# Optimization experiments

Hardware: AMD Instinct MI355X
Metric: run time of the kernel (lower is better)

Reference implementation:

```python
import jax, jax.numpy as jnp
from jax import lax
import numpy as np

N, H, K, B, L = 8192, 256, 100, 32, 128
FS = [1, 2, 3, 4]
W2 = 2 * H + 10  # conv kernel width; padded input width (2H+10) == kernel width -> out width 1


def setup_inputs() -> dict:
    key = jax.random.key(0)
    ks = jax.random.split(key, 16)
    inp = {}
    # scale adj by 1/sqrt(N) so layer1 activations stay O(1) (keeps softmax numerically sane)
    inp["adj"] = jax.random.normal(ks[0], (N, N), jnp.float32) / np.float32(np.sqrt(N))
    # xavier-uniform-scale init for the node embedding parameter
    inp["embedding"] = jax.random.normal(ks[1], (N, H), jnp.float32) * np.float32(np.sqrt(2.0 / (N + H)))
    inp["q_idx"] = jax.random.randint(ks[2], (B, L), 0, N, dtype=jnp.int32)
    inp["a_idx"] = jax.random.randint(ks[3], (B, L), 0, N, dtype=jnp.int32)
    for i, fs in enumerate(FS):
        fan_in = fs * W2
        inp[f"conv_w{i}"] = jax.random.normal(ks[4 + i], (K, 1, fs, W2), jnp.float32) / np.float32(np.sqrt(fan_in))
        inp[f"conv_b{i}"] = jnp.zeros((K,), jnp.float32)
    inp["dense_w"] = jax.random.normal(ks[12], (4 * K * 2, 2), jnp.float32) * np.float32(0.02)
    inp["dense_b"] = jnp.zeros((2,), jnp.float32)
    return inp


def _cnn_branch(t, conv_ws, conv_bs):
    # t: [B, 1, L, 2H]; each conv has padding=5 on both spatial dims,
    # kernel width == 2H+10 so output width == 1; relu then max-pool over full height.
    outs = []
    for w, b in zip(conv_ws, conv_bs):
        y = lax.conv_general_dilated(t, w, (1, 1), [(5, 5), (5, 5)],
                                     dimension_numbers=("NCHW", "OIHW", "NCHW"))
        y = jax.nn.relu(y + b[None, :, None, None])  # [B, K, L+10-fs+1, 1]
        outs.append(jnp.max(y, axis=(2, 3)))  # [B, K]
    return jnp.concatenate(outs, axis=1)  # [B, 4K]


def reference(adj, embedding, q_idx, a_idx,
              conv_w0, conv_b0, conv_w1, conv_b1,
              conv_w2, conv_b2, conv_w3, conv_b3,
              dense_w, dense_b):
    conv_ws = [conv_w0, conv_w1, conv_w2, conv_w3]
    conv_bs = [conv_b0, conv_b1, conv_b2, conv_b3]
    # featureless GCN layer: layer1 = A @ E  -> [N, H]
    layer1 = adj @ embedding
    # per-sample word gathers (ragged in original, fixed length L here)
    Q = layer1[q_idx]  # [B, L, H]
    A = layer1[a_idx]  # [B, L, H]
    # soft alignment: score = Q A^T; wq = softmax rows; wa = softmax(score.T, dim=1) == softmax over axis 1
    score = jnp.einsum("blh,bmh->blm", Q, A)
    wq = jax.nn.softmax(score, axis=2)
    wa = jax.nn.softmax(score, axis=1)
    EQ = jnp.einsum("blm,bmh->blh", wq, A)  # aligned encoding of Q
    EA = jnp.einsum("blm,blh->bmh", wa, Q)  # aligned encoding of A
    # match features: squared diff ++ elementwise product -> [B, 1, L, 2H]
    tq = jnp.concatenate([(Q - EQ) ** 2, Q * EQ], axis=-1)[:, None]
    ta = jnp.concatenate([(A - EA) ** 2, A * EA], axis=-1)[:, None]
    # dropout is identity in eval mode
    q_re = jax.nn.relu(_cnn_branch(tq, conv_ws, conv_bs))  # [B, 4K]
    a_re = jax.nn.relu(_cnn_branch(ta, conv_ws, conv_bs))  # [B, 4K]
    re = jnp.concatenate([q_re, a_re], axis=1)  # [B, 8K]
    logits = re @ dense_w + dense_b  # [B, 2]  (F.relu(score) in original is a discarded no-op)
    return jax.nn.log_softmax(logits, axis=1)
```

## Files before the change

### kernel.cpp

```cpp
#include <hip/hip_runtime.h>
#include <hip/hip_bf16.h>
#include <stdint.h>

typedef unsigned short u16;
typedef __attribute__((ext_vector_type(8))) short bf16x8;
typedef __attribute__((ext_vector_type(4))) float f32x4;

#define NN 8192
#define HH 256
#define KK 100
#define BB 32
#define LL 128
#define NPAD 1024
#define SPLITK 8
#define KCH (NN / SPLITK)
#define STEPS1 (KCH / 64)
#define STEPS2 (512 / 64)

__device__ __forceinline__ u16 f2bf_rne(float x) {
  union { __hip_bfloat16 h; u16 u; } v;
  v.h = __float2bfloat16(x);
  return v.u;
}

__device__ __forceinline__ float bf2f(u16 u) {
  union { unsigned int i; float f; } v;
  v.i = ((unsigned int)u) << 16;
  return v.f;
}

__device__ __forceinline__ bf16x8 pack8(f32x4 a, f32x4 b) {
  bf16x8 r;
  r[0] = (short)f2bf_rne(a.x); r[1] = (short)f2bf_rne(a.y);
  r[2] = (short)f2bf_rne(a.z); r[3] = (short)f2bf_rne(a.w);
  r[4] = (short)f2bf_rne(b.x); r[5] = (short)f2bf_rne(b.y);
  r[6] = (short)f2bf_rne(b.z); r[7] = (short)f2bf_rne(b.w);
  return r;
}

__device__ __forceinline__ void gld16(const void* g, void* l) {
  __builtin_amdgcn_global_load_lds(
      (const __attribute__((address_space(1))) unsigned int*)g,
      (__attribute__((address_space(3))) unsigned int*)l, 16, 0, 0);
}

__global__ __launch_bounds__(256) void convert_embT(const float* __restrict__ emb,
                                                    u16* __restrict__ embT) {
  __shared__ float t[64][65];
  const int tid = threadIdx.x;
  const int k0 = blockIdx.x * 64, n0 = blockIdx.y * 64;
#pragma unroll
  for (int i = 0; i < 16; ++i) {
    int idx = i * 256 + tid;
    int r = idx >> 6, c = idx & 63;
    t[r][c] = emb[(size_t)(k0 + r) * HH + n0 + c];
  }
  __syncthreads();
#pragma unroll
  for (int i = 0; i < 16; ++i) {
    int idx = i * 256 + tid;
    int r = idx >> 6, c = idx & 63;
    embT[(size_t)(n0 + r) * NN + k0 + c] = f2bf_rne(t[c][r]);
  }
}

__global__ __launch_bounds__(1024) void dedup_rows(const int* __restrict__ q_idx,
                                                   const int* __restrict__ a_idx,
                                                   int* __restrict__ rank,
                                                   int* __restrict__ rows,
                                                   int* __restrict__ muniq) {
  __shared__ unsigned bm[256];
  __shared__ int cnt[1024];
  __shared__ int total;
  const int tid = threadIdx.x;
  if (tid < 256) bm[tid] = 0u;
  __syncthreads();
  for (int i = tid; i < BB * LL; i += 1024) {
    int q = q_idx[i];
    atomicOr(&bm[q >> 5], 1u << (q & 31));
  }
  for (int i = tid; i < BB * LL; i += 1024) {
    int a = a_idx[i];
    atomicOr(&bm[a >> 5], 1u << (a & 31));
  }
  __syncthreads();
  const unsigned w = bm[tid >> 2];
  const unsigned byte = (w >> ((tid & 3) * 8)) & 0xffu;
  const int myc = __popc(byte);
  cnt[tid] = myc;
  __syncthreads();
  for (int off = 1; off < 1024; off <<= 1) {
    int v = (tid >= off) ? cnt[tid - off] : 0;
    __syncthreads();
    cnt[tid] += v;
    __syncthreads();
  }
  if (tid == 1023) total = cnt[1023];
  int base = cnt[tid] - myc;
#pragma unroll
  for (int j = 0; j < 8; ++j) {
    int n = tid * 8 + j;
    int bit = (byte >> j) & 1;
    rank[n] = base;
    if (bit) rows[base++] = n;
  }
  __syncthreads();
  if (tid == 0) *muniq = total;
  if (tid < 128) rows[total + tid] = 0;
}

__global__ __launch_bounds__(512, 6) void gemm_layer1c(const float* __restrict__ adj,
                                                       const u16* __restrict__ embT,
                                                       const int* __restrict__ rows,
                                                       const int* __restrict__ muniq,
                                                       u16* __restrict__ parts) {
  __shared__ __align__(16) float As[64 * 64];
  __shared__ __align__(16) u16 Bs[256 * 64];
  const int tid = threadIdx.x;
  const int lane = tid & 63, wid = tid >> 6;
  const int wm = wid >> 2, wn = wid & 3;
  const int wg = blockIdx.x;
  const int sk = wg & 7;
  const int mt = wg >> 3;
  const int m0 = mt * 64;
  const int M = *muniq;
  if (m0 >= M) return;
  const int kbeg = sk * KCH;

  f32x4 acc[2][4];
  const f32x4 zf = {0.f, 0.f, 0.f, 0.f};
#pragma unroll
  for (int i = 0; i < 2; ++i)
#pragma unroll
    for (int j = 0; j < 4; ++j) acc[i][j] = zf;

  int aRowLoc[2], aGsrc[2];
  const float* aSrc[2];
#pragma unroll
  for (int j = 0; j < 2; ++j) {
    int t = wid * 2 + j;
    aRowLoc[j] = t * 4 + (lane >> 4);
    aGsrc[j] = (lane & 15) ^ (aRowLoc[j] & 15);
    int grow = rows[m0 + aRowLoc[j]];
    aSrc[j] = adj + (size_t)grow * NN + kbeg + aGsrc[j] * 4;
  }
  const u16* bSrc[4];
#pragma unroll
  for (int j = 0; j < 4; ++j) {
    int t = wid * 4 + j;
    int rowB = t * 8 + (lane >> 3);
    int g = (lane & 7) ^ (rowB & 7);
    bSrc[j] = embT + (size_t)rowB * NN + kbeg + g * 8;
  }

  for (int s = 0; s < STEPS1; ++s) {
    const int ks = s * 64;
#pragma unroll
    for (int j = 0; j < 2; ++j)
      gld16(aSrc[j] + ks, (void*)&As[(wid * 2 + j) * 256]);
#pragma unroll
    for (int j = 0; j < 4; ++j)
      gld16(bSrc[j] + ks, (void*)&Bs[(wid * 4 + j) * 512]);
    __syncthreads();
#pragma unroll
    for (int kk = 0; kk < 64; kk += 32) {
      bf16x8 af[2], bfr[4];
      const int g0 = (kk >> 2) + ((lane >> 4) << 1);
#pragma unroll
      for (int mi = 0; mi < 2; ++mi) {
        int row = wm * 32 + mi * 16 + (lane & 15);
        f32x4 p0 = *reinterpret_cast<const f32x4*>(&As[row * 64 + ((g0 ^ (row & 15)) << 2)]);
        f32x4 p1 = *reinterpret_cast<const f32x4*>(&As[row * 64 + (((g0 + 1) ^ (row & 15)) << 2)]);
        af[mi] = pack8(p0, p1);
      }
      const int gb = (kk >> 3) + (lane >> 4);
#pragma unroll
      for (int ni = 0; ni < 4; ++ni) {
        int row = wn * 64 + ni * 16 + (lane & 15);
        bfr[ni] = *reinterpret_cast<const bf16x8*>(&Bs[row * 64 + ((gb ^ (row & 7)) << 3)]);
      }
#pragma unroll
      for (int mi = 0; mi < 2; ++mi)
#pragma unroll
        for (int ni = 0; ni < 4; ++ni)
          acc[mi][ni] = __builtin_amdgcn_mfma_f32_16x16x32_bf16(af[mi], bfr[ni], acc[mi][ni], 0, 0, 0);
    }
    __syncthreads();
  }

  u16* outp = parts + (size_t)sk * ((size_t)NN * HH);
  const int r0 = (lane >> 4) << 2;
  const int coln = wn * 64 + (lane & 15);
#pragma unroll
  for (int mi = 0; mi < 2; ++mi)
#pragma unroll
    for (int ni = 0; ni < 4; ++ni)
#pragma unroll
      for (int r = 0; r < 4; ++r)
        outp[(size_t)(m0 + wm * 32 + mi * 16 + r0 + r) * HH + coln + ni * 16] = f2bf_rne(acc[mi][ni][r]);
}

__global__ __launch_bounds__(256) void gather_qa(const u16* __restrict__ parts,
                                                 const int* __restrict__ q_idx,
                                                 const int* __restrict__ a_idx,
                                                 const int* __restrict__ rank,
                                                 u16* __restrict__ Qbf, u16* __restrict__ Abf) {
  const int rb = blockIdx.x;
  const bool isA = rb >= BB * LL;
  const int r = isA ? rb - BB * LL : rb;
  const int idx = (isA ? a_idx : q_idx)[r];
  const int cidx = rank[idx];
  const int tid = threadIdx.x;
  float s = 0.f;
#pragma unroll
  for (int p = 0; p < SPLITK; ++p)
    s += bf2f(parts[(size_t)p * ((size_t)NN * HH) + (size_t)cidx * HH + tid]);
  (isA ? Abf : Qbf)[(size_t)r * HH + tid] = f2bf_rne(s);
}

__global__ __launch_bounds__(512) void attn_fused(const u16* __restrict__ Qbf,
                                                  const u16* __restrict__ Abf,
                                                  u16* __restrict__ wqbf,
                                                  u16* __restrict__ watbf) {
  __shared__ __align__(16) char lraw[131072];
  u16* Qs = (u16*)lraw;
  u16* As = (u16*)(lraw + 65536);
  float* sc = (float*)lraw;
  const int b = blockIdx.x;
  const int tid = threadIdx.x;
  const int lane = tid & 63, wid = tid >> 6;
  const int wm = wid >> 2, wn = wid & 3;

  const u16* qsrc = Qbf + (size_t)b * (LL * HH);
  const u16* asrc = Abf + (size_t)b * (LL * HH);
#pragma unroll
  for (int i = 0; i < 8; ++i) {
    int gf = i * 512 + tid;
    int l = gf >> 5, g = gf & 31;
    int gp = g ^ (l & 7);
    *reinterpret_cast<bf16x8*>(&Qs[l * 256 + gp * 8]) = *reinterpret_cast<const bf16x8*>(qsrc + l * 256 + g * 8);
    *reinterpret_cast<bf16x8*>(&As[l * 256 + gp * 8]) = *reinterpret_cast<const bf16x8*>(asrc + l * 256 + g * 8);
  }
  __syncthreads();

  f32x4 acc[4][2];
  const f32x4 zf = {0.f, 0.f, 0.f, 0.f};
#pragma unroll
  for (int i = 0; i < 4; ++i)
#pragma unroll
    for (int j = 0; j < 2; ++j) acc[i][j] = zf;

#pragma unroll
  for (int ks = 0; ks < 8; ++ks) {
    bf16x8 af[4], bfr[2];
#pragma unroll
    for (int mi = 0; mi < 4; ++mi) {
      int row = wm * 64 + mi * 16 + (lane & 15);
      int g = ks * 4 + (lane >> 4);
      af[mi] = *reinterpret_cast<const bf16x8*>(&Qs[row * 256 + (g ^ (row & 7)) * 8]);
    }
#pragma unroll
    for (int ni = 0; ni < 2; ++ni) {
      int row = wn * 32 + ni * 16 + (lane & 15);
      int g = ks * 4 + (lane >> 4);
      bfr[ni] = *reinterpret_cast<const bf16x8*>(&As[row * 256 + (g ^ (row & 7)) * 8]);
    }
#pragma unroll
    for (int mi = 0; mi < 4; ++mi)
#pragma unroll
      for (int ni = 0; ni < 2; ++ni)
        acc[mi][ni] = __builtin_amdgcn_mfma_f32_16x16x32_bf16(af[mi], bfr[ni], acc[mi][ni], 0, 0, 0);
  }
  __syncthreads();

  const int r0 = (lane >> 4) << 2;
#pragma unroll
  for (int mi = 0; mi < 4; ++mi)
#pragma unroll
    for (int ni = 0; ni < 2; ++ni) {
      int m = wn * 32 + ni * 16 + (lane & 15);
#pragma unroll
      for (int r = 0; r < 4; ++r) {
        int l = wm * 64 + mi * 16 + r0 + r;
        sc[l * 132 + m] = acc[mi][ni][r];
      }
    }
  __syncthreads();

  {
    const int l = tid >> 2, j = tid & 3;
    const int base = l * 132 + j * 32;
    float mx = -3.4e38f;
#pragma unroll 8
    for (int c = 0; c < 32; ++c) mx = fmaxf(mx, sc[base + c]);
    mx = fmaxf(mx, __shfl_xor(mx, 1));
    mx = fmaxf(mx, __shfl_xor(mx, 2));
    float sum = 0.f;
#pragma unroll 8
    for (int c = 0; c < 32; ++c) sum += expf(sc[base + c] - mx);
    sum += __shfl_xor(sum, 1);
    sum += __shfl_xor(sum, 2);
    float inv = 1.f / sum;
    u16* o = wqbf + (size_t)b * (LL * LL) + l * 128 + j * 32;
#pragma unroll 8
    for (int c = 0; c < 32; ++c) o[c] = f2bf_rne(expf(sc[base + c] - mx) * inv);
  }
  {
    const int m = tid >> 2, j = tid & 3;
    float mx = -3.4e38f;
#pragma unroll 8
    for (int r = 0; r < 32; ++r) mx = fmaxf(mx, sc[(j * 32 + r) * 132 + m]);
    mx = fmaxf(mx, __shfl_xor(mx, 1));
    mx = fmaxf(mx, __shfl_xor(mx, 2));
    float sum = 0.f;
#pragma unroll 8
    for (int r = 0; r < 32; ++r) sum += expf(sc[(j * 32 + r) * 132 + m] - mx);
    sum += __shfl_xor(sum, 1);
    sum += __shfl_xor(sum, 2);
    float inv = 1.f / sum;
    u16* o = watbf + (size_t)b * (LL * LL) + m * 128 + j * 32;
#pragma unroll 8
    for (int r = 0; r < 32; ++r) o[r] = f2bf_rne(expf(sc[(j * 32 + r) * 132 + m] - mx) * inv);
  }
}

__global__ __launch_bounds__(512) void align_mfma(const u16* __restrict__ wqbf,
                                                  const u16* __restrict__ watbf,
                                                  const u16* __restrict__ Qbf,
                                                  const u16* __restrict__ Abf,
                                                  u16* __restrict__ Tbf) {
  __shared__ __align__(16) u16 wsh[128 * 128];
  __shared__ __align__(16) u16 srcT[256 * 140];
  const int bid = blockIdx.x;
  const int side = bid >> 5, b = bid & 31;
  const int tid = threadIdx.x;
  const int lane = tid & 63, wid = tid >> 6;
  const int wm = wid >> 2, wn = wid & 3;

  const u16* wsrc = (side ? watbf : wqbf) + (size_t)b * (LL * LL);
  const u16* ssrc = (side ? Qbf : Abf) + (size_t)b * (LL * HH);
  const u16* msrc = (side ? Abf : Qbf) + (size_t)b * (LL * HH);

#pragma unroll
  for (int i = 0; i < 4; ++i) {
    int gf = i * 512 + tid;
    int row = gf >> 4, g = gf & 15;
    int gp = g ^ (row & 7);
    *reinterpret_cast<bf16x8*>(&wsh[row * 128 + gp * 8]) = *reinterpret_cast<const bf16x8*>(wsrc + row * 128 + g * 8);
  }
#pragma unroll
  for (int i = 0; i < 8; ++i) {
    int gf = i * 512 + tid;
    int j = gf >> 5, g = gf & 31;
    bf16x8 v = *reinterpret_cast<const bf16x8*>(ssrc + j * 256 + g * 8);
#pragma unroll
    for (int e = 0; e < 8; ++e) srcT[(g * 8 + e) * 140 + j] = (u16)v[e];
  }
  __syncthreads();

  f32x4 acc[4][4];
  const f32x4 zf = {0.f, 0.f, 0.f, 0.f};
#pragma unroll
  for (int i = 0; i < 4; ++i)
#pragma unroll
    for (int j = 0; j < 4; ++j) acc[i][j] = zf;

#pragma unroll
  for (int ks = 0; ks < 4; ++ks) {
    bf16x8 af[4], bfr[4];
#pragma unroll
    for (int mi = 0; mi < 4; ++mi) {
      int row = wm * 64 + mi * 16 + (lane & 15);
      int g = ks * 4 + (lane >> 4);
      af[mi] = *reinterpret_cast<const bf16x8*>(&wsh[row * 128 + (g ^ (row & 7)) * 8]);
    }
#pragma unroll
    for (int ni = 0; ni < 4; ++ni) {
      int h = wn * 64 + ni * 16 + (lane & 15);
      int k = ks * 32 + ((lane >> 4) << 3);
      bfr[ni] = *reinterpret_cast<const bf16x8*>(&srcT[h * 140 + k]);
    }
#pragma unroll
    for (int mi = 0; mi < 4; ++mi)
#pragma unroll
      for (int ni = 0; ni < 4; ++ni)
        acc[mi][ni] = __builtin_amdgcn_mfma_f32_16x16x32_bf16(af[mi], bfr[ni], acc[mi][ni], 0, 0, 0);
  }

  u16* outp = Tbf + (size_t)(side * 4096 + b * 128) * 512;
  const int r0 = (lane >> 4) << 2;
#pragma unroll
  for (int mi = 0; mi < 4; ++mi)
#pragma unroll
    for (int ni = 0; ni < 4; ++ni) {
      int h = wn * 64 + ni * 16 + (lane & 15);
#pragma unroll
      for (int r = 0; r < 4; ++r) {
        int i2 = wm * 64 + mi * 16 + r0 + r;
        float mv = bf2f(msrc[(size_t)i2 * HH + h]);
        float e = acc[mi][ni][r];
        float d = mv - e;
        outp[(size_t)i2 * 512 + h] = f2bf_rne(d * d);
        outp[(size_t)i2 * 512 + 256 + h] = f2bf_rne(mv * e);
      }
    }
}

__global__ __launch_bounds__(256) void prep_wcat(const float* __restrict__ w0,
                                                 const float* __restrict__ w1,
                                                 const float* __restrict__ w2,
                                                 const float* __restrict__ w3,
                                                 u16* __restrict__ Wcat) {
  const int kr = blockIdx.x;
  const int tid = threadIdx.x;
  u16* out = Wcat + (size_t)kr * 512;
  if (kr >= KK * 10) {
    out[tid] = 0;
    out[tid + 256] = 0;
    return;
  }
  const int k = kr / 10, s = kr % 10;
  const float* w;
  int r, fs;
  if (s < 1)      { w = w0; r = s;     fs = 1; }
  else if (s < 3) { w = w1; r = s - 1; fs = 2; }
  else if (s < 6) { w = w2; r = s - 3; fs = 3; }
  else            { w = w3; r = s - 6; fs = 4; }
  const float* src = w + ((size_t)k * fs + r) * 522 + 5;
  out[tid] = f2bf_rne(src[tid]);
  out[tid + 256] = f2bf_rne(src[tid + 256]);
}

__global__ __launch_bounds__(512, 4) void gemm_conv(const u16* __restrict__ Tbf,
                                                    const u16* __restrict__ Wcat,
                                                    u16* __restrict__ D) {
  __shared__ __align__(16) u16 As[128 * 64];
  __shared__ __align__(16) u16 Bs[256 * 64];
  const int tid = threadIdx.x;
  const int lane = tid & 63, wid = tid >> 6;
  const int wm = wid >> 2, wn = wid & 3;
  const int m0 = blockIdx.x * 128;
  const int n0 = blockIdx.y * 256;

  f32x4 acc[4][4];
  const f32x4 zf = {0.f, 0.f, 0.f, 0.f};
#pragma unroll
  for (int i = 0; i < 4; ++i)
#pragma unroll
    for (int j = 0; j < 4; ++j) acc[i][j] = zf;

  const int browL = (lane >> 3);
  const int bkL = (lane & 7) << 3;

  for (int s = 0; s < STEPS2; ++s) {
    const int ks = s * 64;
#pragma unroll
    for (int j = 0; j < 2; ++j) {
      int rowA = (wid << 4) + (j << 3) + browL;
      int kA = bkL ^ ((rowA & 7) << 3);
      gld16(Tbf + (size_t)(m0 + rowA) * 512 + ks + kA, (void*)&As[(wid * 2 + j) * 512]);
    }
#pragma unroll
    for (int j = 0; j < 4; ++j) {
      int rowB = (wid << 5) + (j << 3) + browL;
      int kB = bkL ^ ((rowB & 7) << 3);
      gld16(Wcat + (size_t)(n0 + rowB) * 512 + ks + kB, (void*)&Bs[(wid * 4 + j) * 512]);
    }
    __syncthreads();
#pragma unroll
    for (int kk = 0; kk < 64; kk += 32) {
      const int krow = kk + ((lane >> 4) << 3);
      bf16x8 af[4], bfr[4];
#pragma unroll
      for (int mi = 0; mi < 4; ++mi) {
        int row = wm * 64 + mi * 16 + (lane & 15);
        af[mi] = *reinterpret_cast<const bf16x8*>(&As[row * 64 + (krow ^ ((row & 7) << 3))]);
      }
#pragma unroll
      for (int ni = 0; ni < 4; ++ni) {
        int row = wn * 64 + ni * 16 + (lane & 15);
        bfr[ni] = *reinterpret_cast<const bf16x8*>(&Bs[row * 64 + (krow ^ ((row & 7) << 3))]);
      }
#pragma unroll
      for (int mi = 0; mi < 4; ++mi)
#pragma unroll
        for (int ni = 0; ni < 4; ++ni)
          acc[mi][ni] = __builtin_amdgcn_mfma_f32_16x16x32_bf16(af[mi], bfr[ni], acc[mi][ni], 0, 0, 0);
    }
    __syncthreads();
  }

  const int r0 = (lane >> 4) << 2;
  const int coln = n0 + wn * 64 + (lane & 15);
#pragma unroll
  for (int mi = 0; mi < 4; ++mi)
#pragma unroll
    for (int ni = 0; ni < 4; ++ni)
#pragma unroll
      for (int r = 0; r < 4; ++r)
        D[(size_t)(m0 + wm * 64 + mi * 16 + r0 + r) * NPAD + coln + ni * 16] = f2bf_rne(acc[mi][ni][r]);
}

__global__ __launch_bounds__(256) void reduce_conv(const u16* __restrict__ D,
                                                   const float* __restrict__ b0,
                                                   const float* __restrict__ b1,
                                                   const float* __restrict__ b2,
                                                   const float* __restrict__ b3,
                                                   float* __restrict__ re) {
  __shared__ float tile[128][101];
  const int pair = blockIdx.y;
  const int sel = pair >> 5, b = pair & 31;
  const int kc = blockIdx.x;
  const int tid = threadIdx.x;
  const int rowbase = sel * (BB * LL) + b * LL;
  const int c0 = kc * 100;
  for (int idx = tid; idx < 12800; idx += 256) {
    int r = idx / 100, c = idx - r * 100;
    tile[r][c] = bf2f(D[(size_t)(rowbase + r) * NPAD + c0 + c]);
  }
  __syncthreads();
  const int wid = tid >> 6, lane = tid & 63;
  const int offt[4] = {0, 1, 3, 6};
  const int fst[4] = {1, 2, 3, 4};
  for (int o = wid; o < 40; o += 4) {
    const int kk = o >> 2, f = o & 3;
    const int fs = fst[f], off = offt[f];
    const int kg = kc * 10 + kk;
    const float bias = (f == 0 ? b0 : f == 1 ? b1 : f == 2 ? b2 : b3)[kg];
    const int col = kk * 10 + off;
    const int outh = 139 - fs;
    float best = 0.f;
    for (int i = lane; i < outh; i += 64) {
      float s = bias;
#pragma unroll 4
      for (int r = 0; r < 4; ++r) {
        if (r < fs) {
          int j = i + r - 5;
          if (j >= 0 && j < LL) s += tile[j][col + r];
        }
      }
      best = fmaxf(best, s);
    }
    best = fmaxf(best, 0.f);
#pragma unroll
    for (int d = 32; d; d >>= 1) best = fmaxf(best, __shfl_xor(best, d));
    if (lane == 0) re[(size_t)b * 800 + sel * 400 + f * 100 + kg] = best;
  }
}

__global__ __launch_bounds__(64) void dense_logsm(const float* __restrict__ re,
                                                  const float* __restrict__ dw,
                                                  const float* __restrict__ db,
                                                  float* __restrict__ out) {
  const int b = blockIdx.x;
  const int lane = threadIdx.x;
  const float* r = re + (size_t)b * 800;
  float a0 = 0.f, a1 = 0.f;
  for (int j = lane; j < 800; j += 64) {
    float rv = r[j];
    a0 += rv * dw[j * 2];
    a1 += rv * dw[j * 2 + 1];
  }
#pragma unroll
  for (int d = 32; d; d >>= 1) {
    a0 += __shfl_xor(a0, d);
    a1 += __shfl_xor(a1, d);
  }
  if (lane == 0) {
    a0 += db[0];
    a1 += db[1];
    float mx = fmaxf(a0, a1);
    float lse = mx + logf(expf(a0 - mx) + expf(a1 - mx));
    out[b * 2] = a0 - lse;
    out[b * 2 + 1] = a1 - lse;
  }
}

static const size_t OFF_PARTS = 0;
static const size_t OFF_D     = 0;
static const size_t OFF_QBF   = 67108864;
static const size_t OFF_ABF   = OFF_QBF + 2097152;
static const size_t OFF_WQB   = OFF_ABF + 2097152;
static const size_t OFF_WAB   = OFF_WQB + 1048576;
static const size_t OFF_RE    = OFF_WAB + 1048576;
static const size_t OFF_TBF   = OFF_RE + 102400;
static const size_t OFF_WCAT  = OFF_TBF + 8388608;
static const size_t OFF_EMBT  = OFF_WCAT + 1048576;
static const size_t OFF_RANK  = OFF_EMBT + 4194304;
static const size_t OFF_ROWS  = OFF_RANK + 32768;
static const size_t OFF_MUNIQ = OFF_ROWS + 33280;

extern "C" void kernel_launch(void* const* d_in, const int* in_sizes, int n_in,
                              void* d_out, int out_size, void* d_ws, size_t ws_size,
                              hipStream_t stream) {
  (void)in_sizes; (void)n_in; (void)out_size; (void)ws_size;
  const float* adj  = (const float*)d_in[0];
  const float* emb  = (const float*)d_in[1];
  const int* q_idx  = (const int*)d_in[2];
  const int* a_idx  = (const int*)d_in[3];
  const float* cw0 = (const float*)d_in[4];
  const float* cb0 = (const float*)d_in[5];
  const float* cw1 = (const float*)d_in[6];
  const float* cb1 = (const float*)d_in[7];
  const float* cw2 = (const float*)d_in[8];
  const float* cb2 = (const float*)d_in[9];
  const float* cw3 = (const float*)d_in[10];
  const float* cb3 = (const float*)d_in[11];
  const float* dw = (const float*)d_in[12];
  const float* db = (const float*)d_in[13];
  float* out = (float*)d_out;

  char* ws = (char*)d_ws;
  u16* parts   = (u16*)(ws + OFF_PARTS);
  u16* Dbuf    = (u16*)(ws + OFF_D);
  u16* Qbf     = (u16*)(ws + OFF_QBF);
  u16* Abf     = (u16*)(ws + OFF_ABF);
  u16* wqbf    = (u16*)(ws + OFF_WQB);
  u16* watbf   = (u16*)(ws + OFF_WAB);
  float* re    = (float*)(ws + OFF_RE);
  u16* Tbf     = (u16*)(ws + OFF_TBF);
  u16* Wcat    = (u16*)(ws + OFF_WCAT);
  u16* embT    = (u16*)(ws + OFF_EMBT);
  int* rank    = (int*)(ws + OFF_RANK);
  int* rows    = (int*)(ws + OFF_ROWS);
  int* muniq   = (int*)(ws + OFF_MUNIQ);

  convert_embT<<<dim3(128, 4), 256, 0, stream>>>(emb, embT);
  dedup_rows<<<1, 1024, 0, stream>>>(q_idx, a_idx, rank, rows, muniq);
  prep_wcat<<<1024, 256, 0, stream>>>(cw0, cw1, cw2, cw3, Wcat);
  gemm_layer1c<<<128 * SPLITK, 512, 0, stream>>>(adj, embT, rows, muniq, parts);
  gather_qa<<<2 * BB * LL, 256, 0, stream>>>(parts, q_idx, a_idx, rank, Qbf, Abf);
  attn_fused<<<BB, 512, 0, stream>>>(Qbf, Abf, wqbf, watbf);
  align_mfma<<<64, 512, 0, stream>>>(wqbf, watbf, Qbf, Abf, Tbf);
  gemm_conv<<<dim3(64, 4), 512, 0, stream>>>(Tbf, Wcat, Dbuf);
  reduce_conv<<<dim3(10, 64), 256, 0, stream>>>(Dbuf, cb0, cb1, cb2, cb3, re);
  dense_logsm<<<BB, 64, 0, stream>>>(re, dw, db, out);
}
```

Measured before the change: 148.8 us.

## Split layer1 GEMM into 64x128 tiles with 256-thread blocks

The layer1 gather GEMM now splits the 256-wide output into two N-halves, so each block is 4 waves computing a 64x128 tile instead of 8 waves computing 64x256. The grid doubles, and each wave holds a 4x2 MFMA accumulator layout instead of 2x4. This raises block count and cuts LDS per block for better occupancy and load balance. In exchange, every adj A-tile (fp32, the dominant traffic) is now loaded twice, once per N-half.

```diff
diff --git a/kernel.cpp b/kernel.cpp
--- a/kernel.cpp
+++ b/kernel.cpp
@@ -109,40 +109,40 @@
   if (tid < 128) rows[total + tid] = 0;
 }
 
-__global__ __launch_bounds__(512, 6) void gemm_layer1c(const float* __restrict__ adj,
+__global__ __launch_bounds__(256, 5) void gemm_layer1f(const float* __restrict__ adj,
                                                        const u16* __restrict__ embT,
                                                        const int* __restrict__ rows,
                                                        const int* __restrict__ muniq,
                                                        u16* __restrict__ parts) {
   __shared__ __align__(16) float As[64 * 64];
-  __shared__ __align__(16) u16 Bs[256 * 64];
+  __shared__ __align__(16) u16 Bs[128 * 64];
   const int tid = threadIdx.x;
   const int lane = tid & 63, wid = tid >> 6;
-  const int wm = wid >> 2, wn = wid & 3;
   const int wg = blockIdx.x;
   const int sk = wg & 7;
-  const int mt = wg >> 3;
+  const int nt = (wg >> 3) & 1;
+  const int mt = wg >> 4;
   const int m0 = mt * 64;
   const int M = *muniq;
   if (m0 >= M) return;
+  const int n0 = nt * 128;
   const int kbeg = sk * KCH;
 
-  f32x4 acc[2][4];
+  f32x4 acc[4][2];
   const f32x4 zf = {0.f, 0.f, 0.f, 0.f};
 #pragma unroll
-  for (int i = 0; i < 2; ++i)
-#pragma unroll
-    for (int j = 0; j < 4; ++j) acc[i][j] = zf;
-
-  int aRowLoc[2], aGsrc[2];
-  const float* aSrc[2];
-#pragma unroll
-  for (int j = 0; j < 2; ++j) {
-    int t = wid * 2 + j;
-    aRowLoc[j] = t * 4 + (lane >> 4);
-    aGsrc[j] = (lane & 15) ^ (aRowLoc[j] & 15);
-    int grow = rows[m0 + aRowLoc[j]];
-    aSrc[j] = adj + (size_t)grow * NN + kbeg + aGsrc[j] * 4;
+  for (int i = 0; i < 4; ++i)
+#pragma unroll
+    for (int j = 0; j < 2; ++j) acc[i][j] = zf;
+
+  const float* aSrc[4];
+#pragma unroll
+  for (int j = 0; j < 4; ++j) {
+    int t = wid * 4 + j;
+    int rloc = t * 4 + (lane >> 4);
+    int g = (lane & 15) ^ (rloc & 15);
+    int grow = rows[m0 + rloc];
+    aSrc[j] = adj + (size_t)grow * NN + kbeg + g * 4;
   }
   const u16* bSrc[4];
 #pragma unroll
@@ -150,39 +150,38 @@
     int t = wid * 4 + j;
     int rowB = t * 8 + (lane >> 3);
     int g = (lane & 7) ^ (rowB & 7);
-    bSrc[j] = embT + (size_t)rowB * NN + kbeg + g * 8;
+    bSrc[j] = embT + (size_t)(n0 + rowB) * NN + kbeg + g * 8;
   }
 
   for (int s = 0; s < STEPS1; ++s) {
     const int ks = s * 64;
 #pragma unroll
-    for (int j = 0; j < 2; ++j)
-      gld16(aSrc[j] + ks, (void*)&As[(wid * 2 + j) * 256]);
-#pragma unroll
-    for (int j = 0; j < 4; ++j)
+    for (int j = 0; j < 4; ++j) {
+      gld16(aSrc[j] + ks, (void*)&As[(wid * 4 + j) * 256]);
       gld16(bSrc[j] + ks, (void*)&Bs[(wid * 4 + j) * 512]);
+    }
     __syncthreads();
 #pragma unroll
     for (int kk = 0; kk < 64; kk += 32) {
-      bf16x8 af[2], bfr[4];
+      bf16x8 af[4], bfr[2];
       const int g0 = (kk >> 2) + ((lane >> 4) << 1);
 #pragma unroll
-      for (int mi = 0; mi < 2; ++mi) {
-        int row = wm * 32 + mi * 16 + (lane & 15);
+      for (int mi = 0; mi < 4; ++mi) {
+        int row = mi * 16 + (lane & 15);
         f32x4 p0 = *reinterpret_cast<const f32x4*>(&As[row * 64 + ((g0 ^ (row & 15)) << 2)]);
         f32x4 p1 = *reinterpret_cast<const f32x4*>(&As[row * 64 + (((g0 + 1) ^ (row & 15)) << 2)]);
         af[mi] = pack8(p0, p1);
       }
       const int gb = (kk >> 3) + (lane >> 4);
 #pragma unroll
-      for (int ni = 0; ni < 4; ++ni) {
-        int row = wn * 64 + ni * 16 + (lane & 15);
+      for (int ni = 0; ni < 2; ++ni) {
+        int row = wid * 32 + ni * 16 + (lane & 15);
         bfr[ni] = *reinterpret_cast<const bf16x8*>(&Bs[row * 64 + ((gb ^ (row & 7)) << 3)]);
       }
 #pragma unroll
-      for (int mi = 0; mi < 2; ++mi)
-#pragma unroll
-        for (int ni = 0; ni < 4; ++ni)
+      for (int mi = 0; mi < 4; ++mi)
+#pragma unroll
+        for (int ni = 0; ni < 2; ++ni)
           acc[mi][ni] = __builtin_amdgcn_mfma_f32_16x16x32_bf16(af[mi], bfr[ni], acc[mi][ni], 0, 0, 0);
     }
     __syncthreads();
@@ -190,14 +189,14 @@
 
   u16* outp = parts + (size_t)sk * ((size_t)NN * HH);
   const int r0 = (lane >> 4) << 2;
-  const int coln = wn * 64 + (lane & 15);
-#pragma unroll
-  for (int mi = 0; mi < 2; ++mi)
-#pragma unroll
-    for (int ni = 0; ni < 4; ++ni)
+  const int coln = n0 + wid * 32 + (lane & 15);
+#pragma unroll
+  for (int mi = 0; mi < 4; ++mi)
+#pragma unroll
+    for (int ni = 0; ni < 2; ++ni)
 #pragma unroll
       for (int r = 0; r < 4; ++r)
-        outp[(size_t)(m0 + wm * 32 + mi * 16 + r0 + r) * HH + coln + ni * 16] = f2bf_rne(acc[mi][ni][r]);
+        outp[(size_t)(m0 + mi * 16 + r0 + r) * HH + coln + ni * 16] = f2bf_rne(acc[mi][ni][r]);
 }
 
 __global__ __launch_bounds__(256) void gather_qa(const u16* __restrict__ parts,
@@ -628,7 +627,7 @@
   convert_embT<<<dim3(128, 4), 256, 0, stream>>>(emb, embT);
   dedup_rows<<<1, 1024, 0, stream>>>(q_idx, a_idx, rank, rows, muniq);
   prep_wcat<<<1024, 256, 0, stream>>>(cw0, cw1, cw2, cw3, Wcat);
-  gemm_layer1c<<<128 * SPLITK, 512, 0, stream>>>(adj, embT, rows, muniq, parts);
+  gemm_layer1f<<<128 * 2 * SPLITK, 256, 0, stream>>>(adj, embT, rows, muniq, parts);
   gather_qa<<<2 * BB * LL, 256, 0, stream>>>(parts, q_idx, a_idx, rank, Qbf, Abf);
   attn_fused<<<BB, 512, 0, stream>>>(Qbf, Abf, wqbf, watbf);
   align_mfma<<<64, 512, 0, stream>>>(wqbf, watbf, Qbf, Abf, Tbf);
```

After: 153.0 us. 1.03x slower.

## Fuse conv GEMM with shift-sum max-pool reduction via shared memory

Applied to the files above, without the earlier changes.

Merges the conv GEMM and the reduction kernel into one. Each block now computes one 128-row sample tile against a 160-column slice of weights (16 filters × 10 taps), writes the bf16 result into shared memory, and does the shifted row-sum, bias, relu and max-pool in place. This removes the global round-trip of the intermediate D buffer and one kernel launch. In exchange the tile shape changes to 128×160, the grid grows to 448 blocks, and the weight matrix is padded to 1120 rows, so some padded columns are computed and then discarded.

```diff
diff --git a/kernel.cpp b/kernel.cpp
--- a/kernel.cpp
+++ b/kernel.cpp
@@ -11,11 +11,10 @@
 #define KK 100
 #define BB 32
 #define LL 128
-#define NPAD 1024
 #define SPLITK 8
 #define KCH (NN / SPLITK)
 #define STEPS1 (KCH / 64)
-#define STEPS2 (512 / 64)
+#define WCATR 1120
 
 __device__ __forceinline__ u16 f2bf_rne(float x) {
   union { __hip_bfloat16 h; u16 u; } v;
@@ -431,103 +430,94 @@
   out[tid + 256] = f2bf_rne(src[tid + 256]);
 }
 
-__global__ __launch_bounds__(512, 4) void gemm_conv(const u16* __restrict__ Tbf,
-                                                    const u16* __restrict__ Wcat,
-                                                    u16* __restrict__ D) {
-  __shared__ __align__(16) u16 As[128 * 64];
-  __shared__ __align__(16) u16 Bs[256 * 64];
+__global__ __launch_bounds__(512, 4) void gemm_conv_red(const u16* __restrict__ Tbf,
+                                                        const u16* __restrict__ Wcat,
+                                                        const float* __restrict__ b0,
+                                                        const float* __restrict__ b1,
+                                                        const float* __restrict__ b2,
+                                                        const float* __restrict__ b3,
+                                                        float* __restrict__ re) {
+  __shared__ __align__(16) char smem[41472];
+  u16* As = (u16*)smem;
+  u16* Bs = (u16*)(smem + 16384);
+  u16* Dt = (u16*)smem;
   const int tid = threadIdx.x;
   const int lane = tid & 63, wid = tid >> 6;
-  const int wm = wid >> 2, wn = wid & 3;
-  const int m0 = blockIdx.x * 128;
-  const int n0 = blockIdx.y * 256;
-
-  f32x4 acc[4][4];
+  const int wm = wid >> 1, wn = wid & 1;
+  const int bx = blockIdx.x;
+  const int pair = bx / 7, nt = bx % 7;
+  const int sel = pair >> 5, b = pair & 31;
+  const int m0 = pair * 128;
+  const int n0 = nt * 160;
+
+  f32x4 acc[2][5];
   const f32x4 zf = {0.f, 0.f, 0.f, 0.f};
 #pragma unroll
-  for (int i = 0; i < 4; ++i)
-#pragma unroll
-    for (int j = 0; j < 4; ++j) acc[i][j] = zf;
-
-  const int browL = (lane >> 3);
-  const int bkL = (lane & 7) << 3;
-
-  for (int s = 0; s < STEPS2; ++s) {
+  for (int i = 0; i < 2; ++i)
+#pragma unroll
+    for (int j = 0; j < 5; ++j) acc[i][j] = zf;
+
+  for (int s = 0; s < 8; ++s) {
     const int ks = s * 64;
 #pragma unroll
     for (int j = 0; j < 2; ++j) {
-      int rowA = (wid << 4) + (j << 3) + browL;
-      int kA = bkL ^ ((rowA & 7) << 3);
-      gld16(Tbf + (size_t)(m0 + rowA) * 512 + ks + kA, (void*)&As[(wid * 2 + j) * 512]);
-    }
-#pragma unroll
-    for (int j = 0; j < 4; ++j) {
-      int rowB = (wid << 5) + (j << 3) + browL;
-      int kB = bkL ^ ((rowB & 7) << 3);
-      gld16(Wcat + (size_t)(n0 + rowB) * 512 + ks + kB, (void*)&Bs[(wid * 4 + j) * 512]);
+      int t = wid * 2 + j;
+      int rowA = t * 8 + (lane >> 3);
+      int kA = ((lane & 7) ^ (rowA & 7)) << 3;
+      gld16(Tbf + (size_t)(m0 + rowA) * 512 + ks + kA, (void*)&As[t * 512]);
+    }
+    for (int t = wid; t < 20; t += 8) {
+      int rowB = t * 8 + (lane >> 3);
+      int kB = ((lane & 7) ^ (rowB & 7)) << 3;
+      gld16(Wcat + (size_t)(n0 + rowB) * 512 + ks + kB, (void*)&Bs[t * 512]);
     }
     __syncthreads();
 #pragma unroll
     for (int kk = 0; kk < 64; kk += 32) {
-      const int krow = kk + ((lane >> 4) << 3);
-      bf16x8 af[4], bfr[4];
-#pragma unroll
-      for (int mi = 0; mi < 4; ++mi) {
-        int row = wm * 64 + mi * 16 + (lane & 15);
-        af[mi] = *reinterpret_cast<const bf16x8*>(&As[row * 64 + (krow ^ ((row & 7) << 3))]);
+      const int k8 = (kk >> 3) + (lane >> 4);
+      bf16x8 af[2], bfr[5];
+#pragma unroll
+      for (int mi = 0; mi < 2; ++mi) {
+        int row = wm * 32 + mi * 16 + (lane & 15);
+        af[mi] = *reinterpret_cast<const bf16x8*>(&As[row * 64 + ((k8 ^ (row & 7)) << 3)]);
       }
 #pragma unroll
-      for (int ni = 0; ni < 4; ++ni) {
-        int row = wn * 64 + ni * 16 + (lane & 15);
-        bfr[ni] = *reinterpret_cast<const bf16x8*>(&Bs[row * 64 + (krow ^ ((row & 7) << 3))]);
+      for (int ni = 0; ni < 5; ++ni) {
+        int row = wn * 80 + ni * 16 + (lane & 15);
+        bfr[ni] = *reinterpret_cast<const bf16x8*>(&Bs[row * 64 + ((k8 ^ (row & 7)) << 3)]);
       }
 #pragma unroll
-      for (int mi = 0; mi < 4; ++mi)
-#pragma unroll
-        for (int ni = 0; ni < 4; ++ni)
+      for (int mi = 0; mi < 2; ++mi)
+#pragma unroll
+        for (int ni = 0; ni < 5; ++ni)
           acc[mi][ni] = __builtin_amdgcn_mfma_f32_16x16x32_bf16(af[mi], bfr[ni], acc[mi][ni], 0, 0, 0);
     }
     __syncthreads();
   }
 
   const int r0 = (lane >> 4) << 2;
-  const int coln = n0 + wn * 64 + (lane & 15);
-#pragma unroll
-  for (int mi = 0; mi < 4; ++mi)
-#pragma unroll
-    for (int ni = 0; ni < 4; ++ni)
+#pragma unroll
+  for (int mi = 0; mi < 2; ++mi)
+#pragma unroll
+    for (int ni = 0; ni < 5; ++ni) {
+      int col = wn * 80 + ni * 16 + (lane & 15);
 #pragma unroll
       for (int r = 0; r < 4; ++r)
-        D[(size_t)(m0 + wm * 64 + mi * 16 + r0 + r) * NPAD + coln + ni * 16] = f2bf_rne(acc[mi][ni][r]);
-}
-
-__global__ __launch_bounds__(256) void reduce_conv(const u16* __restrict__ D,
-                                                   const float* __restrict__ b0,
-                                                   const float* __restrict__ b1,
-                                                   const float* __restrict__ b2,
-                                                   const float* __restrict__ b3,
-                                                   float* __restrict__ re) {
-  __shared__ float tile[128][101];
-  const int pair = blockIdx.y;
-  const int sel = pair >> 5, b = pair & 31;
-  const int kc = blockIdx.x;
-  const int tid = threadIdx.x;
-  const int rowbase = sel * (BB * LL) + b * LL;
-  const int c0 = kc * 100;
-  for (int idx = tid; idx < 12800; idx += 256) {
-    int r = idx / 100, c = idx - r * 100;
-    tile[r][c] = bf2f(D[(size_t)(rowbase + r) * NPAD + c0 + c]);
-  }
-  __syncthreads();
-  const int wid = tid >> 6, lane = tid & 63;
+        Dt[(wm * 32 + mi * 16 + r0 + r) * 162 + col] = f2bf_rne(acc[mi][ni][r]);
+    }
+  __syncthreads();
+
   const int offt[4] = {0, 1, 3, 6};
   const int fst[4] = {1, 2, 3, 4};
-  for (int o = wid; o < 40; o += 4) {
-    const int kk = o >> 2, f = o & 3;
+#pragma unroll
+  for (int oi = 0; oi < 8; ++oi) {
+    const int o = wid * 8 + oi;
+    const int kl = o >> 2, f = o & 3;
+    const int kglob = nt * 16 + kl;
+    if (kglob >= KK) continue;
     const int fs = fst[f], off = offt[f];
-    const int kg = kc * 10 + kk;
-    const float bias = (f == 0 ? b0 : f == 1 ? b1 : f == 2 ? b2 : b3)[kg];
-    const int col = kk * 10 + off;
+    const float bias = (f == 0 ? b0 : f == 1 ? b1 : f == 2 ? b2 : b3)[kglob];
+    const int col = kl * 10 + off;
     const int outh = 139 - fs;
     float best = 0.f;
     for (int i = lane; i < outh; i += 64) {
@@ -536,7 +526,7 @@
       for (int r = 0; r < 4; ++r) {
         if (r < fs) {
           int j = i + r - 5;
-          if (j >= 0 && j < LL) s += tile[j][col + r];
+          if (j >= 0 && j < LL) s += bf2f(Dt[j * 162 + col + r]);
         }
       }
       best = fmaxf(best, s);
@@ -544,7 +534,7 @@
     best = fmaxf(best, 0.f);
 #pragma unroll
     for (int d = 32; d; d >>= 1) best = fmaxf(best, __shfl_xor(best, d));
-    if (lane == 0) re[(size_t)b * 800 + sel * 400 + f * 100 + kg] = best;
+    if (lane == 0) re[(size_t)b * 800 + sel * 400 + f * 100 + kglob] = best;
   }
 }
 
@@ -577,7 +567,6 @@
 }
 
 static const size_t OFF_PARTS = 0;
-static const size_t OFF_D     = 0;
 static const size_t OFF_QBF   = 67108864;
 static const size_t OFF_ABF   = OFF_QBF + 2097152;
 static const size_t OFF_WQB   = OFF_ABF + 2097152;
@@ -585,7 +574,7 @@
 static const size_t OFF_RE    = OFF_WAB + 1048576;
 static const size_t OFF_TBF   = OFF_RE + 102400;
 static const size_t OFF_WCAT  = OFF_TBF + 8388608;
-static const size_t OFF_EMBT  = OFF_WCAT + 1048576;
+static const size_t OFF_EMBT  = OFF_WCAT + 1146880;
 static const size_t OFF_RANK  = OFF_EMBT + 4194304;
 static const size_t OFF_ROWS  = OFF_RANK + 32768;
 static const size_t OFF_MUNIQ = OFF_ROWS + 33280;
@@ -612,7 +601,6 @@
 
   char* ws = (char*)d_ws;
   u16* parts   = (u16*)(ws + OFF_PARTS);
-  u16* Dbuf    = (u16*)(ws + OFF_D);
   u16* Qbf     = (u16*)(ws + OFF_QBF);
   u16* Abf     = (u16*)(ws + OFF_ABF);
   u16* wqbf    = (u16*)(ws + OFF_WQB);
@@ -627,12 +615,11 @@
 
   convert_embT<<<dim3(128, 4), 256, 0, stream>>>(emb, embT);
   dedup_rows<<<1, 1024, 0, stream>>>(q_idx, a_idx, rank, rows, muniq);
-  prep_wcat<<<1024, 256, 0, stream>>>(cw0, cw1, cw2, cw3, Wcat);
+  prep_wcat<<<WCATR, 256, 0, stream>>>(cw0, cw1, cw2, cw3, Wcat);
   gemm_layer1c<<<128 * SPLITK, 512, 0, stream>>>(adj, embT, rows, muniq, parts);
   gather_qa<<<2 * BB * LL, 256, 0, stream>>>(parts, q_idx, a_idx, rank, Qbf, Abf);
   attn_fused<<<BB, 512, 0, stream>>>(Qbf, Abf, wqbf, watbf);
   align_mfma<<<64, 512, 0, stream>>>(wqbf, watbf, Qbf, Abf, Tbf);
-  gemm_conv<<<dim3(64, 4), 512, 0, stream>>>(Tbf, Wcat, Dbuf);
-  reduce_conv<<<dim3(10, 64), 256, 0, stream>>>(Dbuf, cb0, cb1, cb2, cb3, re);
+  gemm_conv_red<<<448, 512, 0, stream>>>(Tbf, Wcat, cb0, cb1, cb2, cb3, re);
   dense_logsm<<<BB, 64, 0, stream>>>(re, dw, db, out);
 }
```

Measured after the change: 132.2 us. 11.2% less time.
